# Kernel tuning notes

Hardware: AMD Instinct MI355X
Metric: run time of the kernel (lower is better)

## Reference

```python
import jax, jax.numpy as jnp
import numpy as np

D = 1024
H = 16
HD = D // H
EPS = 1e-6


def setup_inputs() -> dict:
    key = jax.random.key(0)
    ks = jax.random.split(key, 10)
    s = 1.0 / np.sqrt(D)
    inp = {
        "x": jax.random.normal(ks[0], (2, 2048, D), dtype=jnp.float32),
        "Wq": jax.random.uniform(ks[1], (D, D), jnp.float32, -s, s),
        "bq": jax.random.uniform(ks[2], (D,), jnp.float32, -s, s),
        "Wk": jax.random.uniform(ks[3], (D, D), jnp.float32, -s, s),
        "bk": jax.random.uniform(ks[4], (D,), jnp.float32, -s, s),
        "Wv": jax.random.uniform(ks[5], (D, D), jnp.float32, -s, s),
        "bv": jax.random.uniform(ks[6], (D,), jnp.float32, -s, s),
        "Wo": jax.random.uniform(ks[7], (D, D), jnp.float32, -s, s),
        "bo": jax.random.uniform(ks[8], (D,), jnp.float32, -s, s),
        "gamma": jnp.ones((D,), jnp.float32),
        "beta": jnp.zeros((D,), jnp.float32),
    }
    return inp


def _mha(x, Wq, bq, Wk, bk, Wv, bv, Wo, bo, gamma, beta):
    B, S, _ = x.shape
    # Linear projections (torch Linear: x @ W.T + b), split heads -> [B,H,S,hd]
    q = (x @ Wq.T + bq).reshape(B, S, H, HD).transpose(0, 2, 1, 3)
    k = (x @ Wk.T + bk).reshape(B, S, H, HD).transpose(0, 2, 1, 3)
    v = (x @ Wv.T + bv).reshape(B, S, H, HD).transpose(0, 2, 1, 3)
    scores = jnp.einsum("bhqd,bhkd->bhqk", q, k) / jnp.sqrt(jnp.float32(HD))
    attn = jax.nn.softmax(scores, axis=-1)
    ctx = jnp.einsum("bhqk,bhkd->bhqd", attn, v)
    ctx = ctx.transpose(0, 2, 1, 3).reshape(B, S, D)
    out = ctx @ Wo.T + bo  # dropout p=0.0 -> identity
    res = x + out
    mu = jnp.mean(res, axis=-1, keepdims=True)
    var = jnp.mean(jnp.square(res - mu), axis=-1, keepdims=True)
    return (res - mu) / jnp.sqrt(var + EPS) * gamma + beta


def reference(x, Wq, bq, Wk, bk, Wv, bv, Wo, bo, gamma, beta):
    return _mha(x, Wq, bq, Wk, bk, Wv, bv, Wo, bo, gamma, beta)
```

## Files before the change

kernel.cpp:

```cpp
#include <hip/hip_runtime.h>
#include <hip/hip_bf16.h>
#include <math.h>

#define D_MODEL 1024
#define NH 16
#define HDIM 64
#define BB 2
#define SS 2048
#define MTOK (BB*SS)

typedef __hip_bfloat16 bf16;
typedef short s8v __attribute__((ext_vector_type(8)));
typedef float f4v __attribute__((ext_vector_type(4)));
typedef float f16v __attribute__((ext_vector_type(16)));

__device__ __forceinline__ float bf2f(bf16 x) { return __bfloat162float(x); }
__device__ __forceinline__ bf16 f2bf(float x) { return __float2bfloat16(x); }

typedef const __attribute__((address_space(1))) unsigned int* gas_u32;
typedef __attribute__((address_space(3))) unsigned int* las_u32;
#define ASYNC16(gp, lp) __builtin_amdgcn_global_load_lds((gas_u32)(gp), (las_u32)(lp), 16, 0, 0)

#define QSCALE 0.18033688f

__device__ __forceinline__ unsigned int pack_bf16(float a, float b) {
    unsigned int ua = __builtin_bit_cast(unsigned int, a);
    unsigned int ub = __builtin_bit_cast(unsigned int, b);
    return ((ua + 0x8000u) >> 16) | ((ub + 0x8000u) & 0xffff0000u);
}

__global__ __launch_bounds__(256)
void cvt_kernel(const float* __restrict__ x,  const float* __restrict__ wq,
                const float* __restrict__ wk, const float* __restrict__ wv,
                const float* __restrict__ wo, bf16* __restrict__ dst)
{
    const size_t e = ((size_t)blockIdx.x * 256 + threadIdx.x) * 4;
    const size_t M1 = (size_t)1 << 20;
    const float* src; size_t off;
    if      (e < 4 * M1) { src = x;  off = e;          }
    else if (e < 5 * M1) { src = wq; off = e - 4 * M1; }
    else if (e < 6 * M1) { src = wk; off = e - 5 * M1; }
    else if (e < 7 * M1) { src = wv; off = e - 6 * M1; }
    else                 { src = wo; off = e - 7 * M1; }
    const float4 v = *(const float4*)&src[off];
    bf16 h[4] = { f2bf(v.x), f2bf(v.y), f2bf(v.z), f2bf(v.w) };
    *(uint2*)&dst[e] = *(const uint2*)h;
}

__global__ __launch_bounds__(256, 2)
void gemm_qkv(const bf16* __restrict__ X,
              const bf16* __restrict__ Wq, const float* __restrict__ bq,
              const bf16* __restrict__ Wk, const float* __restrict__ bk,
              const bf16* __restrict__ Wv, const float* __restrict__ bv,
              bf16* __restrict__ q_ws, bf16* __restrict__ k_ws, bf16* __restrict__ v_ws)
{
    const int mat = blockIdx.z;
    const bf16*  W    = (mat == 0) ? Wq : ((mat == 1) ? Wk : Wv);
    const float* bias = (mat == 0) ? bq : ((mat == 1) ? bk : bv);

    const int t = threadIdx.x;
    const int lane = t & 63, wave = t >> 6;
    const int wrow = wave >> 1, wcol = wave & 1;
    const int quad = lane >> 4, l15 = lane & 15;

    const bf16 *Ap, *Bp; int m0, n0;
    if (mat < 2) { Ap = X; Bp = W; m0 = blockIdx.y * 128; n0 = blockIdx.x * 128; }
    else         { Ap = W; Bp = X; m0 = blockIdx.x * 128; n0 = blockIdx.y * 128; }

    __shared__ __align__(16) bf16 As[128 * 32];
    __shared__ __align__(16) bf16 Bs[128 * 32];

    f4v acc[4][4];
#pragma unroll
    for (int i = 0; i < 4; i++)
#pragma unroll
        for (int j = 0; j < 4; j++) acc[i][j] = (f4v){0.f, 0.f, 0.f, 0.f};

    const int arow = t >> 2;
    const int acol = (t & 3) * 8;

    for (int kk = 0; kk < D_MODEL; kk += 32) {
        ASYNC16(&Ap[(size_t)(m0 + arow) * D_MODEL + kk + acol],      &As[arow * 32 + acol]);
        ASYNC16(&Ap[(size_t)(m0 + 64 + arow) * D_MODEL + kk + acol], &As[(64 + arow) * 32 + acol]);
        ASYNC16(&Bp[(size_t)(n0 + arow) * D_MODEL + kk + acol],      &Bs[arow * 32 + acol]);
        ASYNC16(&Bp[(size_t)(n0 + 64 + arow) * D_MODEL + kk + acol], &Bs[(64 + arow) * 32 + acol]);
        __syncthreads();

        s8v af[4], bf_[4];
#pragma unroll
        for (int i = 0; i < 4; i++)
            af[i] = *(const s8v*)&As[(wrow * 64 + i * 16 + l15) * 32 + quad * 8];
#pragma unroll
        for (int j = 0; j < 4; j++)
            bf_[j] = *(const s8v*)&Bs[(wcol * 64 + j * 16 + l15) * 32 + quad * 8];
#pragma unroll
        for (int i = 0; i < 4; i++)
#pragma unroll
            for (int j = 0; j < 4; j++)
                acc[i][j] = __builtin_amdgcn_mfma_f32_16x16x32_bf16(af[i], bf_[j], acc[i][j], 0, 0, 0);
        __syncthreads();
    }

    if (mat == 2) {
#pragma unroll
        for (int i = 0; i < 4; i++) {
#pragma unroll
            for (int r = 0; r < 4; r++) {
                const int f = m0 + wrow * 64 + i * 16 + quad * 4 + r;
                const float bv_ = bias[f];
#pragma unroll
                for (int j = 0; j < 4; j++) {
                    const int tok = n0 + wcol * 64 + j * 16 + l15;
                    const int b = tok >> 11, s = tok & 2047;
                    v_ws[((size_t)(b * D_MODEL + f)) * SS + s] = f2bf(acc[i][j][r] + bv_);
                }
            }
        }
    } else {
        bf16* dst = (mat == 0) ? q_ws : k_ws;
        const float scale = (mat == 0) ? QSCALE : 1.0f;
#pragma unroll
        for (int j = 0; j < 4; j++) {
            const int col = n0 + wcol * 64 + j * 16 + l15;
            const float bv_ = bias[col];
            const int h = col >> 6, hd = col & 63;
#pragma unroll
            for (int i = 0; i < 4; i++) {
#pragma unroll
                for (int r = 0; r < 4; r++) {
                    const int row = m0 + wrow * 64 + i * 16 + quad * 4 + r;
                    const int b = row >> 11, s = row & 2047;
                    const float v = (acc[i][j][r] + bv_) * scale;
                    dst[(((size_t)(b * NH + h)) * SS + s) * HDIM + hd] = f2bf(v);
                }
            }
        }
    }
}

__global__ __launch_bounds__(512, 2)
void attn_kernel(const bf16* __restrict__ Q, const bf16* __restrict__ K,
                 const bf16* __restrict__ VtG, bf16* __restrict__ ctx)
{
    const int bh = blockIdx.y;
    const int q0 = blockIdx.x * 256;
    const bf16* Qp = Q   + (size_t)bh * SS * HDIM;
    const bf16* Kp = K   + (size_t)bh * SS * HDIM;
    const bf16* Vp = VtG + (size_t)bh * HDIM * SS;

    __shared__ __align__(16) bf16 Qs[256 * 64];
    __shared__ __align__(16) bf16 Ks[128 * 64];
    __shared__ __align__(16) bf16 Vt[64 * 128];

    const int t = threadIdx.x;
    const int lane = t & 63, wave = t >> 6;
    const int l31 = lane & 31, L5 = lane >> 5;
    const int qb = wave * 32;

#pragma unroll
    for (int p = 0; p < 4; p++) {
        const int c = p * 512 + t;
        const int row = c >> 3, g = (c & 7) ^ (row & 7);
        *(uint4*)&Qs[row * 64 + g * 8] = *(const uint4*)&Qp[(size_t)(q0 + row) * HDIM + (c & 7) * 8];
    }
    __syncthreads();
    s8v qf[4];
#pragma unroll
    for (int kc = 0; kc < 4; kc++) {
        const int g = (kc * 2 + L5) ^ (l31 & 7);
        qf[kc] = *(const s8v*)&Qs[(qb + l31) * 64 + g * 8];
    }

    float l_own = 0.f;
    f16v o_acc[2];
#pragma unroll
    for (int i = 0; i < 16; i++) { o_acc[0][i] = 0.f; o_acc[1][i] = 0.f; }

    for (int s0 = 0; s0 < SS; s0 += 128) {
        __syncthreads();
#pragma unroll
        for (int p = 0; p < 2; p++) {
            const int c = p * 512 + t;
            const int row = c >> 3, g = (c & 7) ^ (row & 7);
            *(uint4*)&Ks[row * 64 + g * 8] = *(const uint4*)&Kp[(size_t)(s0 + row) * HDIM + (c & 7) * 8];
        }
#pragma unroll
        for (int p = 0; p < 2; p++) {
            const int cc = p * 512 + t;
            const int row = cc >> 4, col8 = (cc & 15) * 8;
            union { uint4 u4; uint2 u2[2]; } vv;
            vv.u4 = *(const uint4*)&Vp[(size_t)row * SS + s0 + col8];
            const int cA = col8,     pA = (cA & ~12) | ((cA & 4) << 1) | ((cA & 8) >> 1);
            const int cB = col8 + 4, pB = (cB & ~12) | ((cB & 4) << 1) | ((cB & 8) >> 1);
            *(uint2*)&Vt[row * 128 + (((pA >> 3) ^ (row & 15)) * 8) + (pA & 7)] = vv.u2[0];
            *(uint2*)&Vt[row * 128 + (((pB >> 3) ^ (row & 15)) * 8) + (pB & 7)] = vv.u2[1];
        }
        __syncthreads();

#pragma unroll
        for (int mt = 0; mt < 4; mt++) {
            f16v sc;
#pragma unroll
            for (int i = 0; i < 16; i++) sc[i] = 0.f;
#pragma unroll
            for (int kc = 0; kc < 4; kc++) {
                const int g = (kc * 2 + L5) ^ (l31 & 7);
                const s8v kf = *(const s8v*)&Ks[(mt * 32 + l31) * 64 + g * 8];
                sc = __builtin_amdgcn_mfma_f32_32x32x16_bf16(kf, qf[kc], sc, 0, 0, 0);
            }
            float tps = 0.f;
#pragma unroll
            for (int i = 0; i < 16; i++) { sc[i] = __builtin_amdgcn_exp2f(sc[i]); tps += sc[i]; }
            l_own += tps;
            unsigned int pk[8];
#pragma unroll
            for (int i = 0; i < 8; i++) pk[i] = pack_bf16(sc[2 * i], sc[2 * i + 1]);
#pragma unroll
            for (int c = 0; c < 2; c++) {
                const s8v pf = *(const s8v*)&pk[c * 4];
#pragma unroll
                for (int dt = 0; dt < 2; dt++) {
                    const int g = (mt * 4 + c * 2 + L5) ^ (l31 & 15);
                    const s8v vf = *(const s8v*)&Vt[(dt * 32 + l31) * 128 + g * 8];
                    o_acc[dt] = __builtin_amdgcn_mfma_f32_32x32x16_bf16(pf, vf, o_acc[dt], 0, 0, 0);
                }
            }
        }
    }

    const float l_full = l_own + __shfl_xor(l_own, 32);
    const float linv = 1.0f / l_full;
    const int b = bh >> 4, h = bh & 15;
#pragma unroll
    for (int reg = 0; reg < 16; reg++) {
        const int R = (reg & 3) + 8 * (reg >> 2) + 4 * L5;
        const float lr = __shfl(linv, R);
        const int tok = q0 + qb + R;
        const size_t rb = ((size_t)(b * SS + tok)) * D_MODEL + h * 64;
        ctx[rb + l31]      = f2bf(o_acc[0][reg] * lr);
        ctx[rb + 32 + l31] = f2bf(o_acc[1][reg] * lr);
    }
}

__global__ __launch_bounds__(256, 2)
void gemm_oproj(const bf16* __restrict__ Ctx, const bf16* __restrict__ Wo,
                const float* __restrict__ bo, const float* __restrict__ X,
                float* __restrict__ res)
{
    const int m0 = blockIdx.y * 128, n0 = blockIdx.x * 128;
    const int t = threadIdx.x;
    const int lane = t & 63, wave = t >> 6;
    const int wrow = wave >> 1, wcol = wave & 1;
    const int quad = lane >> 4, l15 = lane & 15;

    __shared__ __align__(16) bf16 As[128 * 32];
    __shared__ __align__(16) bf16 Bs[128 * 32];

    f4v acc[4][4];
#pragma unroll
    for (int i = 0; i < 4; i++)
#pragma unroll
        for (int j = 0; j < 4; j++) acc[i][j] = (f4v){0.f, 0.f, 0.f, 0.f};

    const int arow = t >> 2;
    const int acol = (t & 3) * 8;

    for (int kk = 0; kk < D_MODEL; kk += 32) {
        ASYNC16(&Ctx[(size_t)(m0 + arow) * D_MODEL + kk + acol],      &As[arow * 32 + acol]);
        ASYNC16(&Ctx[(size_t)(m0 + 64 + arow) * D_MODEL + kk + acol], &As[(64 + arow) * 32 + acol]);
        ASYNC16(&Wo[(size_t)(n0 + arow) * D_MODEL + kk + acol],       &Bs[arow * 32 + acol]);
        ASYNC16(&Wo[(size_t)(n0 + 64 + arow) * D_MODEL + kk + acol],  &Bs[(64 + arow) * 32 + acol]);
        __syncthreads();

        s8v af[4], bf_[4];
#pragma unroll
        for (int i = 0; i < 4; i++)
            af[i] = *(const s8v*)&As[(wrow * 64 + i * 16 + l15) * 32 + quad * 8];
#pragma unroll
        for (int j = 0; j < 4; j++)
            bf_[j] = *(const s8v*)&Bs[(wcol * 64 + j * 16 + l15) * 32 + quad * 8];
#pragma unroll
        for (int i = 0; i < 4; i++)
#pragma unroll
            for (int j = 0; j < 4; j++)
                acc[i][j] = __builtin_amdgcn_mfma_f32_16x16x32_bf16(af[i], bf_[j], acc[i][j], 0, 0, 0);
        __syncthreads();
    }

#pragma unroll
    for (int j = 0; j < 4; j++) {
        const int col = n0 + wcol * 64 + j * 16 + l15;
        const float bv_ = bo[col];
#pragma unroll
        for (int i = 0; i < 4; i++) {
#pragma unroll
            for (int r = 0; r < 4; r++) {
                const int row = m0 + wrow * 64 + i * 16 + quad * 4 + r;
                const size_t idx = (size_t)row * D_MODEL + col;
                res[idx] = acc[i][j][r] + bv_ + X[idx];
            }
        }
    }
}

__global__ __launch_bounds__(256)
void ln_kernel(const float* __restrict__ res, const float* __restrict__ gamma,
               const float* __restrict__ beta, float* __restrict__ out)
{
    const int row = blockIdx.x;
    const int t = threadIdx.x;
    const float4 v = *(const float4*)&res[(size_t)row * D_MODEL + t * 4];

    float s = v.x + v.y + v.z + v.w;
    float sq = v.x * v.x + v.y * v.y + v.z * v.z + v.w * v.w;
#pragma unroll
    for (int m = 1; m < 64; m <<= 1) {
        s += __shfl_xor(s, m);
        sq += __shfl_xor(sq, m);
    }
    __shared__ float red[8];
    const int wave = t >> 6, lane = t & 63;
    if (lane == 0) { red[wave] = s; red[4 + wave] = sq; }
    __syncthreads();
    s = red[0] + red[1] + red[2] + red[3];
    sq = red[4] + red[5] + red[6] + red[7];
    const float mu = s * (1.0f / D_MODEL);
    const float var = sq * (1.0f / D_MODEL) - mu * mu;
    const float rstd = rsqrtf(var + 1e-6f);

    const float vv[4] = {v.x, v.y, v.z, v.w};
    float4 o;
    o.x = (vv[0] - mu) * rstd * gamma[t * 4 + 0] + beta[t * 4 + 0];
    o.y = (vv[1] - mu) * rstd * gamma[t * 4 + 1] + beta[t * 4 + 1];
    o.z = (vv[2] - mu) * rstd * gamma[t * 4 + 2] + beta[t * 4 + 2];
    o.w = (vv[3] - mu) * rstd * gamma[t * 4 + 3] + beta[t * 4 + 3];
    *(float4*)&out[(size_t)row * D_MODEL + t * 4] = o;
}

extern "C" void kernel_launch(void* const* d_in, const int* in_sizes, int n_in,
                              void* d_out, int out_size, void* d_ws, size_t ws_size,
                              hipStream_t stream) {
    const float* x     = (const float*)d_in[0];
    const float* Wq    = (const float*)d_in[1];
    const float* bq    = (const float*)d_in[2];
    const float* Wk    = (const float*)d_in[3];
    const float* bk    = (const float*)d_in[4];
    const float* Wv    = (const float*)d_in[5];
    const float* bv    = (const float*)d_in[6];
    const float* Wo    = (const float*)d_in[7];
    const float* bo    = (const float*)d_in[8];
    const float* gamma = (const float*)d_in[9];
    const float* beta  = (const float*)d_in[10];
    float* out = (float*)d_out;

    char* ws = (char*)d_ws;
    bf16* xb  = (bf16*)(ws);
    bf16* Wqb = (bf16*)(ws + ((size_t)8 << 20));
    bf16* Wkb = (bf16*)(ws + ((size_t)10 << 20));
    bf16* Wvb = (bf16*)(ws + ((size_t)12 << 20));
    bf16* Wob = (bf16*)(ws + ((size_t)14 << 20));
    bf16*  q_ws   = (bf16*)(ws + ((size_t)16 << 20));
    bf16*  k_ws   = (bf16*)(ws + ((size_t)24 << 20));
    bf16*  v_ws   = (bf16*)(ws + ((size_t)32 << 20));
    bf16*  ctx_ws = (bf16*)(ws + ((size_t)40 << 20));
    float* res_ws = (float*)(ws + ((size_t)16 << 20));

    cvt_kernel<<<8192, 256, 0, stream>>>(x, Wq, Wk, Wv, Wo, xb);
    gemm_qkv<<<dim3(8, 32, 3), 256, 0, stream>>>(xb, Wqb, bq, Wkb, bk, Wvb, bv, q_ws, k_ws, v_ws);
    attn_kernel<<<dim3(8, 32), 512, 0, stream>>>(q_ws, k_ws, v_ws, ctx_ws);
    gemm_oproj<<<dim3(8, 32), 256, 0, stream>>>(ctx_ws, Wob, bo, x, res_ws);
    ln_kernel<<<MTOK, 256, 0, stream>>>(res_ws, gamma, beta, out);
}
```

Before: 212.4 us.

## Double-buffer K/V tiles in attention with async LDS loads and MFMA priority

Converts the attention inner loop to a double-buffered pipeline: the next K tile is fetched directly into LDS with global_load_lds while the current tile is computed, and the next V tile is loaded into registers early and written to the alternate LDS buffer after compute. This cuts the two barriers per iteration to one and hides global latency behind MFMA work. It also raises wave priority around the MFMA blocks with s_setprio. LDS use grows (K and V buffers doubled, roughly 64KB total), which may limit occupancy at 2 blocks of 512 threads per CU.

```diff
diff --git a/kernel.cpp b/kernel.cpp
--- a/kernel.cpp
+++ b/kernel.cpp
@@ -149,21 +149,43 @@
     const bf16* Vp = VtG + (size_t)bh * HDIM * SS;
 
     __shared__ __align__(16) bf16 Qs[256 * 64];
-    __shared__ __align__(16) bf16 Ks[128 * 64];
-    __shared__ __align__(16) bf16 Vt[64 * 128];
+    __shared__ __align__(16) bf16 Ks[2][128 * 64];
+    __shared__ __align__(16) bf16 Vt[2][64 * 128];
 
     const int t = threadIdx.x;
     const int lane = t & 63, wave = t >> 6;
     const int l31 = lane & 31, L5 = lane >> 5;
     const int qb = wave * 32;
 
+    const int vrow0 = t >> 4,          vcol0 = (t & 15) * 8;
+    const int vrow1 = (512 + t) >> 4,  vcol1 = (t & 15) * 8;
+    uint4 vv0 = *(const uint4*)&Vp[(size_t)vrow0 * SS + vcol0];
+    uint4 vv1 = *(const uint4*)&Vp[(size_t)vrow1 * SS + vcol1];
+#pragma unroll
+    for (int p = 0; p < 2; p++) {
+        const int c = p * 512 + t;
+        const int row = c >> 3, j = c & 7;
+        ASYNC16(&Kp[(size_t)row * HDIM + (j ^ (row & 7)) * 8], &Ks[0][c * 8]);
+    }
 #pragma unroll
     for (int p = 0; p < 4; p++) {
         const int c = p * 512 + t;
         const int row = c >> 3, g = (c & 7) ^ (row & 7);
         *(uint4*)&Qs[row * 64 + g * 8] = *(const uint4*)&Qp[(size_t)(q0 + row) * HDIM + (c & 7) * 8];
     }
+    {
+        union { uint4 u4; uint2 u2[2]; } uu;
+        const int cA0 = vcol0,     pA0 = (cA0 & ~12) | ((cA0 & 4) << 1) | ((cA0 & 8) >> 1);
+        const int cB0 = vcol0 + 4, pB0 = (cB0 & ~12) | ((cB0 & 4) << 1) | ((cB0 & 8) >> 1);
+        uu.u4 = vv0;
+        *(uint2*)&Vt[0][vrow0 * 128 + (((pA0 >> 3) ^ (vrow0 & 15)) * 8) + (pA0 & 7)] = uu.u2[0];
+        *(uint2*)&Vt[0][vrow0 * 128 + (((pB0 >> 3) ^ (vrow0 & 15)) * 8) + (pB0 & 7)] = uu.u2[1];
+        uu.u4 = vv1;
+        *(uint2*)&Vt[0][vrow1 * 128 + (((pA0 >> 3) ^ (vrow1 & 15)) * 8) + (pA0 & 7)] = uu.u2[0];
+        *(uint2*)&Vt[0][vrow1 * 128 + (((pB0 >> 3) ^ (vrow1 & 15)) * 8) + (pB0 & 7)] = uu.u2[1];
+    }
     __syncthreads();
+
     s8v qf[4];
 #pragma unroll
     for (int kc = 0; kc < 4; kc++) {
@@ -176,38 +198,39 @@
 #pragma unroll
     for (int i = 0; i < 16; i++) { o_acc[0][i] = 0.f; o_acc[1][i] = 0.f; }
 
-    for (int s0 = 0; s0 < SS; s0 += 128) {
-        __syncthreads();
-#pragma unroll
-        for (int p = 0; p < 2; p++) {
-            const int c = p * 512 + t;
-            const int row = c >> 3, g = (c & 7) ^ (row & 7);
-            *(uint4*)&Ks[row * 64 + g * 8] = *(const uint4*)&Kp[(size_t)(s0 + row) * HDIM + (c & 7) * 8];
-        }
-#pragma unroll
-        for (int p = 0; p < 2; p++) {
-            const int cc = p * 512 + t;
-            const int row = cc >> 4, col8 = (cc & 15) * 8;
-            union { uint4 u4; uint2 u2[2]; } vv;
-            vv.u4 = *(const uint4*)&Vp[(size_t)row * SS + s0 + col8];
-            const int cA = col8,     pA = (cA & ~12) | ((cA & 4) << 1) | ((cA & 8) >> 1);
-            const int cB = col8 + 4, pB = (cB & ~12) | ((cB & 4) << 1) | ((cB & 8) >> 1);
-            *(uint2*)&Vt[row * 128 + (((pA >> 3) ^ (row & 15)) * 8) + (pA & 7)] = vv.u2[0];
-            *(uint2*)&Vt[row * 128 + (((pB >> 3) ^ (row & 15)) * 8) + (pB & 7)] = vv.u2[1];
-        }
-        __syncthreads();
-
+    int cur = 0;
+    for (int it = 0; it < SS / 128; ++it) {
+        const bool have = (it < SS / 128 - 1);
+        const int s0n = (it + 1) * 128;
+
+        uint4 nv0, nv1;
+        if (have) {
+            nv0 = *(const uint4*)&Vp[(size_t)vrow0 * SS + s0n + vcol0];
+            nv1 = *(const uint4*)&Vp[(size_t)vrow1 * SS + s0n + vcol1];
+#pragma unroll
+            for (int p = 0; p < 2; p++) {
+                const int c = p * 512 + t;
+                const int row = c >> 3, j = c & 7;
+                ASYNC16(&Kp[(size_t)(s0n + row) * HDIM + (j ^ (row & 7)) * 8],
+                        &Ks[cur ^ 1][c * 8]);
+            }
+        }
+
+        const bf16* Ksc = &Ks[cur][0];
+        const bf16* Vtc = &Vt[cur][0];
 #pragma unroll
         for (int mt = 0; mt < 4; mt++) {
             f16v sc;
 #pragma unroll
             for (int i = 0; i < 16; i++) sc[i] = 0.f;
+            __builtin_amdgcn_s_setprio(1);
 #pragma unroll
             for (int kc = 0; kc < 4; kc++) {
                 const int g = (kc * 2 + L5) ^ (l31 & 7);
-                const s8v kf = *(const s8v*)&Ks[(mt * 32 + l31) * 64 + g * 8];
+                const s8v kf = *(const s8v*)&Ksc[(mt * 32 + l31) * 64 + g * 8];
                 sc = __builtin_amdgcn_mfma_f32_32x32x16_bf16(kf, qf[kc], sc, 0, 0, 0);
             }
+            __builtin_amdgcn_s_setprio(0);
             float tps = 0.f;
 #pragma unroll
             for (int i = 0; i < 16; i++) { sc[i] = __builtin_amdgcn_exp2f(sc[i]); tps += sc[i]; }
@@ -215,17 +238,34 @@
             unsigned int pk[8];
 #pragma unroll
             for (int i = 0; i < 8; i++) pk[i] = pack_bf16(sc[2 * i], sc[2 * i + 1]);
+            __builtin_amdgcn_s_setprio(1);
 #pragma unroll
             for (int c = 0; c < 2; c++) {
                 const s8v pf = *(const s8v*)&pk[c * 4];
 #pragma unroll
                 for (int dt = 0; dt < 2; dt++) {
                     const int g = (mt * 4 + c * 2 + L5) ^ (l31 & 15);
-                    const s8v vf = *(const s8v*)&Vt[(dt * 32 + l31) * 128 + g * 8];
+                    const s8v vf = *(const s8v*)&Vtc[(dt * 32 + l31) * 128 + g * 8];
                     o_acc[dt] = __builtin_amdgcn_mfma_f32_32x32x16_bf16(pf, vf, o_acc[dt], 0, 0, 0);
                 }
             }
-        }
+            __builtin_amdgcn_s_setprio(0);
+        }
+
+        if (have) {
+            bf16* VtN = &Vt[cur ^ 1][0];
+            union { uint4 u4; uint2 u2[2]; } uu;
+            const int cA = vcol0,     pA = (cA & ~12) | ((cA & 4) << 1) | ((cA & 8) >> 1);
+            const int cB = vcol0 + 4, pB = (cB & ~12) | ((cB & 4) << 1) | ((cB & 8) >> 1);
+            uu.u4 = nv0;
+            *(uint2*)&VtN[vrow0 * 128 + (((pA >> 3) ^ (vrow0 & 15)) * 8) + (pA & 7)] = uu.u2[0];
+            *(uint2*)&VtN[vrow0 * 128 + (((pB >> 3) ^ (vrow0 & 15)) * 8) + (pB & 7)] = uu.u2[1];
+            uu.u4 = nv1;
+            *(uint2*)&VtN[vrow1 * 128 + (((pA >> 3) ^ (vrow1 & 15)) * 8) + (pA & 7)] = uu.u2[0];
+            *(uint2*)&VtN[vrow1 * 128 + (((pB >> 3) ^ (vrow1 & 15)) * 8) + (pB & 7)] = uu.u2[1];
+        }
+        __syncthreads();
+        cur ^= 1;
     }
 
     const float l_full = l_own + __shfl_xor(l_own, 32);
```

New measurement: 212.1 us. Within noise of the previous version (-0.1%).
